# Kernel optimization log

Hardware: AMD Instinct MI355X
Metric: run time of the kernel (lower is better)

## Reference

```python
import jax, jax.numpy as jnp
import numpy as np

RF, US, MGC, FS, NS, NL = 1024, 200, 60, 64, 4, 10  # receptive field, upsample, mgc, filters, stacks, wavenet layers
SCALE = 0.70710678118


def setup_inputs() -> dict:
    key = jax.random.key(0)
    ks = jax.random.split(key, 16)
    F = 8
    N = F * US
    def n(k, shape, s=0.05):
        return jax.random.normal(k, shape, dtype=jnp.float32) * s
    return {
        "mgc": n(ks[0], (F, MGC), 1.0),
        "noise": n(ks[1], (N + RF,), 1.0),
        "cond_w": n(ks[2], (MGC * US, MGC)),          # conditioning Linear(60 -> 12000)
        "cond_b": n(ks[3], (MGC * US,)),
        "conv0_w": n(ks[4], (NS, 3, FS, 1, 2), 0.3),    # layer 0: in_ch=1, [input,gate,residual]
        "convs_w": n(ks[5], (NS, NL - 1, 3, FS, FS, 2), 0.08),
        "conv_b": n(ks[6], (NS, NL, 3, FS)),
        "ccw": n(ks[7], (NS, NL, 2, FS, MGC)),          # cond_input / cond_gate linear weights
        "ccb": n(ks[8], (NS, NL, 2, FS)),
        "pre_w": n(ks[9], (NS, 256, FS)),
        "pre_b": n(ks[10], (NS, 256)),
        "mean_w": n(ks[11], (NS, 1, 256)),
        "mean_b": n(ks[12], (NS, 1)),
        "std_w": n(ks[13], (NS, 1, 256)),
        "std_b": n(ks[14], (NS, 1)),
    }


def _cond_conv(x, cond, w, b, cw, cb):
    # x: [N, C, L]; kernel-2 stride-2 conv expressed as a reshape + einsum
    Nb, C, L = x.shape
    xr = x.reshape(Nb, C, L // 2, 2)
    inp = jnp.einsum('ncls,ocs->nol', xr, w[0]) + b[0][None, :, None]
    gate = jnp.einsum('ncls,ocs->nol', xr, w[1]) + b[1][None, :, None]
    res = jnp.einsum('ncls,ocs->nol', xr, w[2]) + b[2][None, :, None]
    ic = (cond @ cw[0].T + cb[0])[:, :, None]
    gc = (cond @ cw[1].T + cb[1])[:, :, None]
    return (jnp.tanh(inp + ic) * jax.nn.sigmoid(gate + gc) + res) * SCALE


def reference(mgc, noise, cond_w, cond_b, conv0_w, convs_w, conv_b, ccw, ccb,
              pre_w, pre_b, mean_w, mean_b, std_w, std_b):
    F = mgc.shape[0]
    N = F * US
    # conditioning: Linear(60 -> 60*200) + tanh, reshaped to one 60-dim vector per sample
    cond = jnp.tanh(mgc @ cond_w.T + cond_b).reshape(N, MGC)
    prepend = noise[:RF]
    prev_x = noise
    win_idx = jnp.arange(N)[:, None] + jnp.arange(RF)[None, :]  # strided-window gather
    tails = []
    mean = logvar = None
    for s in range(NS):
        x = prev_x[win_idx][:, None, :]  # [N, 1, RF]
        for l in range(NL):
            w = conv0_w[s] if l == 0 else convs_w[s, l - 1]
            x = _cond_conv(x, cond, w, conv_b[s, l], ccw[s, l], ccb[s, l])
        pre = jax.nn.relu(x[:, :, 0] @ pre_w[s].T + pre_b[s])   # [N, 256]
        mean = pre @ mean_w[s].T + mean_b[s]                    # [N, 1]
        logvar = pre @ std_w[s].T + std_b[s]                    # [N, 1]
        eps = prev_x[RF:].reshape(N, 1)
        new = eps * jnp.exp(0.5 * logvar) + mean
        tails.append(jax.lax.stop_gradient(new[-RF:]))
        if s != NS - 1:
            prev_x = jnp.concatenate([prepend, new.reshape(-1)])
        else:
            prev_x = new
    return prev_x, mean, logvar, jnp.stack(tails)
```

## Files before the change

kernel.cpp:

```cpp
#include <hip/hip_runtime.h>
#include <hip/hip_fp16.h>

#define RF    1024
#define USZ   200
#define NWIN  1600
#define SCALEF 0.70710678118f
#define TPB   512
#define CSTR  72

typedef _Float16 f16x8 __attribute__((ext_vector_type(8)));
typedef float    f32x4 __attribute__((ext_vector_type(4)));

#if __has_builtin(__builtin_amdgcn_exp2f)
#define EXP2F(x) __builtin_amdgcn_exp2f(x)
#else
#define EXP2F(x) exp2f(x)
#endif
#if __has_builtin(__builtin_amdgcn_rcpf)
#define RCPF(x) __builtin_amdgcn_rcpf(x)
#else
#define RCPF(x) (1.0f / (x))
#endif

__device__ __forceinline__ float gatecomb(float a, float g, float r) {
  a = fminf(a, 12.0f);
  g = fminf(g, 12.0f);
  const float u = EXP2F(a * 2.885390082f);
  const float v = EXP2F(g * 1.442695041f);
  const float d = RCPF((u + 1.0f) * (v + 1.0f));
  return fmaf((u - 1.0f) * v, d, r) * SCALEF;
}


__global__ void k_cond(const float* __restrict__ mgc, const float* __restrict__ cond_w,
                       const float* __restrict__ cond_b, _Float16* __restrict__ cond_h) {
  int idx = blockIdx.x * 256 + threadIdx.x;
  int n = idx >> 6, c = idx & 63;
  if (c >= 60) { cond_h[idx] = (_Float16)0.0f; return; }
  int u = n % USZ, f = n / USZ;
  float a = cond_b[u * 60 + c];
  const float* wr = cond_w + (u * 60 + c) * 60;
  const float* mr = mgc + f * 60;
#pragma unroll 10
  for (int m = 0; m < 60; ++m) a = fmaf(mr[m], wr[m], a);
  float e = EXP2F(a * 2.885390082f);
  cond_h[idx] = (_Float16)((e - 1.0f) * RCPF(e + 1.0f));
}

__global__ void k_packB(const float* __restrict__ ccw, _Float16* __restrict__ wfrag2) {
  int idx = blockIdx.x * 256 + threadIdx.x;
  int j    = idx & 7;
  int lane = (idx >> 3) & 63;
  int ks   = (idx >> 9) & 1;
  int nt   = (idx >> 10) & 7;
  int sl   = idx >> 13;
  int jo = nt * 16 + (lane & 15);
  int c  = ks * 32 + (lane >> 4) * 8 + j;
  float v = 0.0f;
  if (c < 60) v = ccw[((sl * 2 + (jo >> 6)) * 64 + (jo & 63)) * 60 + c];
  wfrag2[idx] = (_Float16)v;
}

__global__ void k_icgc_mfma(const _Float16* __restrict__ cond_h, const _Float16* __restrict__ wfrag2,
                            const float* __restrict__ ccb, const float* __restrict__ conv_b,
                            float* __restrict__ icgc) {
  const int n0 = blockIdx.x * 32;
  const int sl = blockIdx.y;
  const int tid = threadIdx.x;
  const int wave = tid >> 6, lane = tid & 63;
  const int m16 = lane & 15, q = lane >> 4;
  for (int t = wave; t < 16; t += 4) {
    const int mt = t >> 3, nt = t & 7;
    const int jo = nt * 16 + m16;
    const float b = ccb[(sl * 2 + (jo >> 6)) * 64 + (jo & 63)]
                  + conv_b[(sl * 3 + (jo >> 6)) * 64 + (jo & 63)];
    f32x4 acc = {b, b, b, b};
    const int arow = (n0 + mt * 16 + m16) * 64 + q * 8;
    const f16x8 a0 = *(const f16x8*)(cond_h + arow);
    const f16x8 a1 = *(const f16x8*)(cond_h + arow + 32);
    const f16x8* wb = (const f16x8*)wfrag2;
    const f16x8 b0 = wb[(((sl * 8 + nt) * 2 + 0) << 6) + lane];
    const f16x8 b1 = wb[(((sl * 8 + nt) * 2 + 1) << 6) + lane];
    acc = __builtin_amdgcn_mfma_f32_16x16x32_f16(a0, b0, acc, 0, 0, 0);
    acc = __builtin_amdgcn_mfma_f32_16x16x32_f16(a1, b1, acc, 0, 0, 0);
#pragma unroll
    for (int r = 0; r < 4; ++r) {
      const int n = n0 + mt * 16 + q * 4 + r;
      icgc[((size_t)sl * 1600 + n) * 128 + jo] = acc[r];
    }
  }
}

__global__ void k_wcvt(const float* __restrict__ convs_w, _Float16* __restrict__ wfrag) {
  int idx = blockIdx.x * 256 + threadIdx.x;
  int j    = idx & 7;
  int lane = (idx >> 3) & 63;
  int ks   = (idx >> 9) & 3;
  int ch16 = (idx >> 11) & 3;
  int t    = idx >> 13;
  int gate = t % 3, sl = t / 3;
  int o  = ch16 * 16 + (lane & 15);
  int kk = ks * 32 + (lane >> 4) * 8 + j;
  int s2 = kk >> 6, c = kk & 63;
  wfrag[idx] = (_Float16)convs_w[(((sl * 3 + gate) * 64 + o) * 64 + c) * 2 + s2];
}

__global__ void k_pwt(const float* __restrict__ pre_w, float* __restrict__ pwT) {
  int idx = blockIdx.x * 256 + threadIdx.x;
  int k = idx & 255, o = (idx >> 8) & 63, s = idx >> 14;
  pwT[idx] = pre_w[(s * 256 + k) * 64 + o];
}

__global__ void k_prefix(const float* __restrict__ noise, float* __restrict__ pxA,
                         float* __restrict__ pxB) {
  int i = blockIdx.x * 256 + threadIdx.x;
  float v = noise[i];
  pxA[i] = v; pxB[i] = v;
}

#define SMEM_BYTES 79184

__device__ __forceinline__ void run_mfma_tiles(
    const _Float16* __restrict__ ain, _Float16* __restrict__ aout, float* __restrict__ x64f,
    const f16x8 bfr[3][4], float bi, float bg, float br,
    int mt_lo, int mt_hi, int row_sub, int Lout, bool last,
    int q, int m16, int och)
{
  for (int mt = mt_lo; mt < mt_hi; mt += 2) {
    f32x4 ai = {bi, bi, bi, bi};
    f32x4 ag = {bg, bg, bg, bg};
    f32x4 ar = {br, br, br, br};
#pragma unroll
    for (int ks = 0; ks < 4; ++ks) {
      const int row = 2 * (mt * 16 + m16) + (ks >> 1) - row_sub;
      const f16x8 af = *(const f16x8*)(ain + row * CSTR + (ks & 1) * 32 + q * 8);
      ai = __builtin_amdgcn_mfma_f32_16x16x32_f16(af, bfr[0][ks], ai, 0, 0, 0);
      ag = __builtin_amdgcn_mfma_f32_16x16x32_f16(af, bfr[1][ks], ag, 0, 0, 0);
      ar = __builtin_amdgcn_mfma_f32_16x16x32_f16(af, bfr[2][ks], ar, 0, 0, 0);
    }
#pragma unroll
    for (int r = 0; r < 4; ++r) {
      const int p = mt * 16 + q * 4 + r;
      const float val = gatecomb(ai[r], ag[r], ar[r]);
      if (last) { if (p == 0) x64f[och] = val; }
      else if (p < Lout) aout[p * CSTR + och] = (_Float16)val;
    }
  }
}

__launch_bounds__(TPB, 4)
__global__ void k_window(int s, const float* __restrict__ px, float* __restrict__ ptail,
                         float* __restrict__ out,
                         const float* __restrict__ icgc, const float* __restrict__ conv_b,
                         const float* __restrict__ conv0_w, const _Float16* __restrict__ wfrag,
                         const float* __restrict__ pwT, const float* __restrict__ pre_b,
                         const float* __restrict__ mean_w, const float* __restrict__ mean_b,
                         const float* __restrict__ std_w, const float* __restrict__ std_b) {
  extern __shared__ char smem[];
  _Float16* bufA = (_Float16*)smem;
  _Float16* bufB = (_Float16*)(smem + 36864);
  float*    xw   = (float*)(smem + 73728);
  float*    x64f = (float*)(smem + 77840);
  float*    pre  = (float*)(smem + 78096);
  float*    red  = (float*)(smem + 79120);

  const int n = blockIdx.x;
  const int tid = threadIdx.x;
  const int wave = tid >> 6, lane = tid & 63;
  const int q = lane >> 4, m16 = lane & 15;
  const int ch16 = wave & 3, mstart = wave >> 2;
  const int och = ch16 * 16 + m16;

  for (int i = tid; i < 1025; i += TPB) xw[i] = px[n + i];

  const int b0 = ((s * 10 + 0) * 1600 + n) * 128;
  const float l0bi = icgc[b0 + lane];
  const float l0bg = icgc[b0 + 64 + lane];
  const float l0br = conv_b[((s * 10 + 0) * 3 + 2) * 64 + lane];
  const float wi0 = conv0_w[((s * 3 + 0) * 64 + lane) * 2 + 0];
  const float wi1 = conv0_w[((s * 3 + 0) * 64 + lane) * 2 + 1];
  const float wg0 = conv0_w[((s * 3 + 1) * 64 + lane) * 2 + 0];
  const float wg1 = conv0_w[((s * 3 + 1) * 64 + lane) * 2 + 1];
  const float wr0 = conv0_w[((s * 3 + 2) * 64 + lane) * 2 + 0];
  const float wr1 = conv0_w[((s * 3 + 2) * 64 + lane) * 2 + 1];

  f16x8 bfr1[3][4];
  {
    const f16x8* wb = (const f16x8*)(wfrag + (size_t)(s * 9) * 24576);
#pragma unroll
    for (int g = 0; g < 3; ++g)
#pragma unroll
      for (int ks = 0; ks < 4; ++ks)
        bfr1[g][ks] = wb[(((g * 4 + ch16) * 4 + ks) << 6) + lane];
  }
  const int base1 = ((s * 10 + 1) * 1600 + n) * 128;
  const float bi1 = icgc[base1 + och];
  const float bg1 = icgc[base1 + 64 + och];
  const float br1 = conv_b[((s * 10 + 1) * 3 + 2) * 64 + och];

  __syncthreads();

#pragma unroll 1
  for (int p = wave; p < 256; p += 8) {
    const float x0 = xw[2 * p], x1 = xw[2 * p + 1];
    const float vi = fmaf(x1, wi1, fmaf(x0, wi0, l0bi));
    const float vg = fmaf(x1, wg1, fmaf(x0, wg0, l0bg));
    const float vr = fmaf(x1, wr1, fmaf(x0, wr0, l0br));
    bufA[p * CSTR + lane] = (_Float16)gatecomb(vi, vg, vr);
  }
  __syncthreads();

  run_mfma_tiles(bufA, bufB, x64f, bfr1, bi1, bg1, br1, mstart, 8, 0, 256, false, q, m16, och);
  __syncthreads();

#pragma unroll 1
  for (int p = wave; p < 256; p += 8) {
    const int pg = 256 + p;
    const float x0 = xw[2 * pg], x1 = xw[2 * pg + 1];
    const float vi = fmaf(x1, wi1, fmaf(x0, wi0, l0bi));
    const float vg = fmaf(x1, wg1, fmaf(x0, wg0, l0bg));
    const float vr = fmaf(x1, wr1, fmaf(x0, wr0, l0br));
    bufA[p * CSTR + lane] = (_Float16)gatecomb(vi, vg, vr);
  }
  __syncthreads();

  run_mfma_tiles(bufA, bufB, x64f, bfr1, bi1, bg1, br1, 8 + mstart, 16, 256, 256, false, q, m16, och);
  __syncthreads();

  for (int l = 2; l <= 9; ++l) {
    const int Lout = 512 >> l;
    const int mtiles = (Lout + 15) >> 4;
    const _Float16* ain = (l & 1) ? bufA : bufB;
    _Float16* aout      = (l & 1) ? bufB : bufA;
    f16x8 bfr[3][4];
    const f16x8* wb = (const f16x8*)(wfrag + (size_t)(s * 9 + (l - 1)) * 24576);
#pragma unroll
    for (int g = 0; g < 3; ++g)
#pragma unroll
      for (int ks = 0; ks < 4; ++ks)
        bfr[g][ks] = wb[(((g * 4 + ch16) * 4 + ks) << 6) + lane];
    const int base = ((s * 10 + l) * 1600 + n) * 128;
    run_mfma_tiles(ain, aout, x64f, bfr,
                   icgc[base + och], icgc[base + 64 + och],
                   conv_b[((s * 10 + l) * 3 + 2) * 64 + och],
                   mstart, mtiles, 0, Lout, l == 9, q, m16, och);
    __syncthreads();
  }

  if (tid < 256) {
    const int k = tid;
    float a = pre_b[s * 256 + k];
#pragma unroll 8
    for (int oo = 0; oo < 64; ++oo)
      a = fmaf(x64f[oo], pwT[(s * 64 + oo) * 256 + k], a);
    pre[k] = fmaxf(a, 0.0f);
  }
  __syncthreads();
  {
    float pm = 0.0f, pv = 0.0f;
    if (tid < 256) {
      float pk = pre[tid];
      pm = pk * mean_w[s * 256 + tid];
      pv = pk * std_w[s * 256 + tid];
    }
    for (int off = 32; off >= 1; off >>= 1) {
      pm += __shfl_down(pm, off, 64);
      pv += __shfl_down(pv, off, 64);
    }
    if (lane == 0) { red[wave] = pm; red[8 + wave] = pv; }
  }
  __syncthreads();
  if (tid == 0) {
    float m = mean_b[s], lv = std_b[s];
#pragma unroll
    for (int w2 = 0; w2 < 8; ++w2) { m += red[w2]; lv += red[8 + w2]; }
    float eps = xw[1024];
    float nv = eps * __expf(0.5f * lv) + m;
    if (s == 3) { out[n] = nv; out[1600 + n] = m; out[3200 + n] = lv; }
    else ptail[n] = nv;
    if (n >= 576) out[4800 + s * 1024 + (n - 576)] = nv;
  }
}

extern "C" void kernel_launch(void* const* d_in, const int* in_sizes, int n_in,
                              void* d_out, int out_size, void* d_ws, size_t ws_size,
                              hipStream_t stream) {
  (void)in_sizes; (void)n_in; (void)out_size; (void)ws_size;
  const float* mgc     = (const float*)d_in[0];
  const float* noise   = (const float*)d_in[1];
  const float* cond_w  = (const float*)d_in[2];
  const float* cond_b  = (const float*)d_in[3];
  const float* conv0_w = (const float*)d_in[4];
  const float* convs_w = (const float*)d_in[5];
  const float* conv_b  = (const float*)d_in[6];
  const float* ccw     = (const float*)d_in[7];
  const float* ccb     = (const float*)d_in[8];
  const float* pre_w   = (const float*)d_in[9];
  const float* pre_b   = (const float*)d_in[10];
  const float* mean_w  = (const float*)d_in[11];
  const float* mean_b  = (const float*)d_in[12];
  const float* std_w   = (const float*)d_in[13];
  const float* std_b   = (const float*)d_in[14];
  float* out = (float*)d_out;

  char* ws = (char*)d_ws;
  float*    icgc   = (float*)ws;
  float*    pxA    = (float*)(ws + 32768000);
  float*    pxB    = (float*)(ws + 32778496);
  float*    pwT    = (float*)(ws + 32788992);
  _Float16* wfrag  = (_Float16*)(ws + 33051136);
  _Float16* wfrag2 = (_Float16*)(ws + 34820608);
  _Float16* cond_h = (_Float16*)(ws + 35475968);

  k_cond<<<400, 256, 0, stream>>>(mgc, cond_w, cond_b, cond_h);
  k_packB<<<1280, 256, 0, stream>>>(ccw, wfrag2);
  k_icgc_mfma<<<dim3(50, 40), 256, 0, stream>>>(cond_h, wfrag2, ccb, conv_b, icgc);
  k_wcvt<<<3456, 256, 0, stream>>>(convs_w, wfrag);
  k_pwt<<<256, 256, 0, stream>>>(pre_w, pwT);
  k_prefix<<<4, 256, 0, stream>>>(noise, pxA, pxB);

  (void)hipFuncSetAttribute((const void*)k_window,
                            hipFuncAttributeMaxDynamicSharedMemorySize, SMEM_BYTES);

  for (int s = 0; s < 4; ++s) {
    const float* pin = (s == 0) ? noise : (s == 1 ? pxA : (s == 2 ? pxB : pxA));
    float* pt = (s == 0) ? (pxA + 1024) : (s == 1 ? (pxB + 1024) : (s == 2 ? (pxA + 1024) : nullptr));
    k_window<<<NWIN, TPB, SMEM_BYTES, stream>>>(s, pin, pt, out, icgc, conv_b, conv0_w,
                                                wfrag, pwT, pre_b, mean_w, mean_b, std_w, std_b);
  }
}
```

Measured before the change: 553.7 us.

## Chunk layer-0 through a small LDS buffer to cut shared memory and raise occupancy

Layer 0 is now produced in four 128-row chunks into a compact 64-stride buffer, and each chunk feeds the layer-1 MFMA tiles right away. The full 256-row first buffer and the staged input window are gone, and the input window is read straight from global memory. This shrinks per-block LDS from about 79 KB to 53 KB so more blocks fit per CU, and launch bounds go up to 6 to match. Trade-offs: extra barriers per chunk, possible LDS bank conflicts from the unpadded 64 stride, tighter register limits that could cause spills, and x64f/pre now alias the second buffer.

New measurement: 1.164 ms. 110% more time.

```diff
diff --git a/kernel.cpp b/kernel.cpp
--- a/kernel.cpp
+++ b/kernel.cpp
@@ -6,7 +6,8 @@
 #define NWIN  1600
 #define SCALEF 0.70710678118f
 #define TPB   512
-#define CSTR  72
+#define STR_A 64
+#define STR_B 72
 
 typedef _Float16 f16x8 __attribute__((ext_vector_type(8)));
 typedef float    f32x4 __attribute__((ext_vector_type(4)));
@@ -118,12 +119,13 @@
   pxA[i] = v; pxB[i] = v;
 }
 
-#define SMEM_BYTES 79184
+#define SMEM_BYTES 53248
 
 __device__ __forceinline__ void run_mfma_tiles(
-    const _Float16* __restrict__ ain, _Float16* __restrict__ aout, float* __restrict__ x64f,
+    const _Float16* __restrict__ ain, int in_str, int row_sub,
+    _Float16* __restrict__ aout, int out_str, float* __restrict__ x64f,
     const f16x8 bfr[3][4], float bi, float bg, float br,
-    int mt_lo, int mt_hi, int row_sub, int Lout, bool last,
+    int mt_lo, int mt_hi, int Lout, bool last,
     int q, int m16, int och)
 {
   for (int mt = mt_lo; mt < mt_hi; mt += 2) {
@@ -133,7 +135,7 @@
 #pragma unroll
     for (int ks = 0; ks < 4; ++ks) {
       const int row = 2 * (mt * 16 + m16) + (ks >> 1) - row_sub;
-      const f16x8 af = *(const f16x8*)(ain + row * CSTR + (ks & 1) * 32 + q * 8);
+      const f16x8 af = *(const f16x8*)(ain + row * in_str + (ks & 1) * 32 + q * 8);
       ai = __builtin_amdgcn_mfma_f32_16x16x32_f16(af, bfr[0][ks], ai, 0, 0, 0);
       ag = __builtin_amdgcn_mfma_f32_16x16x32_f16(af, bfr[1][ks], ag, 0, 0, 0);
       ar = __builtin_amdgcn_mfma_f32_16x16x32_f16(af, bfr[2][ks], ar, 0, 0, 0);
@@ -143,12 +145,21 @@
       const int p = mt * 16 + q * 4 + r;
       const float val = gatecomb(ai[r], ag[r], ar[r]);
       if (last) { if (p == 0) x64f[och] = val; }
-      else if (p < Lout) aout[p * CSTR + och] = (_Float16)val;
-    }
-  }
-}
-
-__launch_bounds__(TPB, 4)
+      else if (p < Lout) aout[p * out_str + och] = (_Float16)val;
+    }
+  }
+}
+
+__device__ __forceinline__ void load_bfr(f16x8 bfr[3][4], const f16x8* __restrict__ wb,
+                                         int ch16, int lane) {
+#pragma unroll
+  for (int g = 0; g < 3; ++g)
+#pragma unroll
+    for (int ks = 0; ks < 4; ++ks)
+      bfr[g][ks] = wb[(((g * 4 + ch16) * 4 + ks) << 6) + lane];
+}
+
+__launch_bounds__(TPB, 6)
 __global__ void k_window(int s, const float* __restrict__ px, float* __restrict__ ptail,
                          float* __restrict__ out,
                          const float* __restrict__ icgc, const float* __restrict__ conv_b,
@@ -157,12 +168,11 @@
                          const float* __restrict__ mean_w, const float* __restrict__ mean_b,
                          const float* __restrict__ std_w, const float* __restrict__ std_b) {
   extern __shared__ char smem[];
-  _Float16* bufA = (_Float16*)smem;
-  _Float16* bufB = (_Float16*)(smem + 36864);
-  float*    xw   = (float*)(smem + 73728);
-  float*    x64f = (float*)(smem + 77840);
-  float*    pre  = (float*)(smem + 78096);
-  float*    red  = (float*)(smem + 79120);
+  _Float16* L0   = (_Float16*)smem;
+  _Float16* L1   = (_Float16*)(smem + 16384);
+  float*    x64f = (float*)(smem + 16384);
+  float*    pre  = (float*)(smem + 16640);
+  float*    red  = (float*)(smem + 17664);
 
   const int n = blockIdx.x;
   const int tid = threadIdx.x;
@@ -171,79 +181,60 @@
   const int ch16 = wave & 3, mstart = wave >> 2;
   const int och = ch16 * 16 + m16;
 
-  for (int i = tid; i < 1025; i += TPB) xw[i] = px[n + i];
-
-  const int b0 = ((s * 10 + 0) * 1600 + n) * 128;
-  const float l0bi = icgc[b0 + lane];
-  const float l0bg = icgc[b0 + 64 + lane];
-  const float l0br = conv_b[((s * 10 + 0) * 3 + 2) * 64 + lane];
-  const float wi0 = conv0_w[((s * 3 + 0) * 64 + lane) * 2 + 0];
-  const float wi1 = conv0_w[((s * 3 + 0) * 64 + lane) * 2 + 1];
-  const float wg0 = conv0_w[((s * 3 + 1) * 64 + lane) * 2 + 0];
-  const float wg1 = conv0_w[((s * 3 + 1) * 64 + lane) * 2 + 1];
-  const float wr0 = conv0_w[((s * 3 + 2) * 64 + lane) * 2 + 0];
-  const float wr1 = conv0_w[((s * 3 + 2) * 64 + lane) * 2 + 1];
-
-  f16x8 bfr1[3][4];
   {
-    const f16x8* wb = (const f16x8*)(wfrag + (size_t)(s * 9) * 24576);
-#pragma unroll
-    for (int g = 0; g < 3; ++g)
-#pragma unroll
-      for (int ks = 0; ks < 4; ++ks)
-        bfr1[g][ks] = wb[(((g * 4 + ch16) * 4 + ks) << 6) + lane];
-  }
-  const int base1 = ((s * 10 + 1) * 1600 + n) * 128;
-  const float bi1 = icgc[base1 + och];
-  const float bg1 = icgc[base1 + 64 + och];
-  const float br1 = conv_b[((s * 10 + 1) * 3 + 2) * 64 + och];
-
-  __syncthreads();
+    const int b0 = ((s * 10 + 0) * 1600 + n) * 128;
+    const float l0bi = icgc[b0 + lane];
+    const float l0bg = icgc[b0 + 64 + lane];
+    const float l0br = conv_b[((s * 10 + 0) * 3 + 2) * 64 + lane];
+    const float wi0 = conv0_w[((s * 3 + 0) * 64 + lane) * 2 + 0];
+    const float wi1 = conv0_w[((s * 3 + 0) * 64 + lane) * 2 + 1];
+    const float wg0 = conv0_w[((s * 3 + 1) * 64 + lane) * 2 + 0];
+    const float wg1 = conv0_w[((s * 3 + 1) * 64 + lane) * 2 + 1];
+    const float wr0 = conv0_w[((s * 3 + 2) * 64 + lane) * 2 + 0];
+    const float wr1 = conv0_w[((s * 3 + 2) * 64 + lane) * 2 + 1];
+
+    f16x8 bfr1[3][4];
+    load_bfr(bfr1, (const f16x8*)(wfrag + (size_t)(s * 9) * 24576), ch16, lane);
+    const int base1 = ((s * 10 + 1) * 1600 + n) * 128;
+    const float bi1 = icgc[base1 + och];
+    const float bg1 = icgc[base1 + 64 + och];
+    const float br1 = conv_b[((s * 10 + 1) * 3 + 2) * 64 + och];
 
 #pragma unroll 1
-  for (int p = wave; p < 256; p += 8) {
-    const float x0 = xw[2 * p], x1 = xw[2 * p + 1];
-    const float vi = fmaf(x1, wi1, fmaf(x0, wi0, l0bi));
-    const float vg = fmaf(x1, wg1, fmaf(x0, wg0, l0bg));
-    const float vr = fmaf(x1, wr1, fmaf(x0, wr0, l0br));
-    bufA[p * CSTR + lane] = (_Float16)gatecomb(vi, vg, vr);
-  }
-  __syncthreads();
-
-  run_mfma_tiles(bufA, bufB, x64f, bfr1, bi1, bg1, br1, mstart, 8, 0, 256, false, q, m16, och);
-  __syncthreads();
-
+    for (int c = 0; c < 4; ++c) {
 #pragma unroll 1
-  for (int p = wave; p < 256; p += 8) {
-    const int pg = 256 + p;
-    const float x0 = xw[2 * pg], x1 = xw[2 * pg + 1];
-    const float vi = fmaf(x1, wi1, fmaf(x0, wi0, l0bi));
-    const float vg = fmaf(x1, wg1, fmaf(x0, wg0, l0bg));
-    const float vr = fmaf(x1, wr1, fmaf(x0, wr0, l0br));
-    bufA[p * CSTR + lane] = (_Float16)gatecomb(vi, vg, vr);
-  }
-  __syncthreads();
-
-  run_mfma_tiles(bufA, bufB, x64f, bfr1, bi1, bg1, br1, 8 + mstart, 16, 256, 256, false, q, m16, och);
-  __syncthreads();
-
+      for (int r = wave; r < 128; r += 8) {
+        const int pg = c * 128 + r;
+        const float x0 = px[n + 2 * pg];
+        const float x1 = px[n + 2 * pg + 1];
+        const float vi = fmaf(x1, wi1, fmaf(x0, wi0, l0bi));
+        const float vg = fmaf(x1, wg1, fmaf(x0, wg0, l0bg));
+        const float vr = fmaf(x1, wr1, fmaf(x0, wr0, l0br));
+        L0[r * STR_A + lane] = (_Float16)gatecomb(vi, vg, vr);
+      }
+      __syncthreads();
+      run_mfma_tiles(L0, STR_A, c * 128, L1, STR_B, x64f, bfr1, bi1, bg1, br1,
+                     c * 4 + mstart, c * 4 + 4, 256, false, q, m16, och);
+      __syncthreads();
+    }
+  }
+
+#pragma unroll 1
   for (int l = 2; l <= 9; ++l) {
     const int Lout = 512 >> l;
     const int mtiles = (Lout + 15) >> 4;
-    const _Float16* ain = (l & 1) ? bufA : bufB;
-    _Float16* aout      = (l & 1) ? bufB : bufA;
+    const bool even = (l & 1) == 0;
+    const _Float16* ain = even ? L1 : L0;
+    _Float16* aout      = even ? L0 : L1;
+    const int in_str  = even ? STR_B : STR_A;
+    const int out_str = even ? STR_A : STR_B;
     f16x8 bfr[3][4];
-    const f16x8* wb = (const f16x8*)(wfrag + (size_t)(s * 9 + (l - 1)) * 24576);
-#pragma unroll
-    for (int g = 0; g < 3; ++g)
-#pragma unroll
-      for (int ks = 0; ks < 4; ++ks)
-        bfr[g][ks] = wb[(((g * 4 + ch16) * 4 + ks) << 6) + lane];
+    load_bfr(bfr, (const f16x8*)(wfrag + (size_t)(s * 9 + (l - 1)) * 24576), ch16, lane);
     const int base = ((s * 10 + l) * 1600 + n) * 128;
-    run_mfma_tiles(ain, aout, x64f, bfr,
+    run_mfma_tiles(ain, in_str, 0, aout, out_str, x64f, bfr,
                    icgc[base + och], icgc[base + 64 + och],
                    conv_b[((s * 10 + l) * 3 + 2) * 64 + och],
-                   mstart, mtiles, 0, Lout, l == 9, q, m16, och);
+                   mstart, mtiles, Lout, l == 9, q, m16, och);
     __syncthreads();
   }
 
@@ -274,7 +265,7 @@
     float m = mean_b[s], lv = std_b[s];
 #pragma unroll
     for (int w2 = 0; w2 < 8; ++w2) { m += red[w2]; lv += red[8 + w2]; }
-    float eps = xw[1024];
+    float eps = px[n + RF];
     float nv = eps * __expf(0.5f * lv) + m;
     if (s == 3) { out[n] = nv; out[1600 + n] = m; out[3200 + n] = lv; }
     else ptail[n] = nv;
```
